# Kernel optimization log

Measured on AMD Instinct MI355X. Metric: run time of the kernel, lower is better.

The kernel has to match this reference:

```python
import jax, jax.numpy as jnp
import numpy as np

RESO = 128

def _prefix_a3(layer, off0):
    # a3[0]=off0; a3[i]=a3[i-1]+2*layer[i-1]+2*layer[i]
    t = jnp.concatenate([jnp.zeros((1,), layer.dtype), 2.0 * layer[:-1] + 2.0 * layer[1:]])
    return off0 + jnp.cumsum(t)

def _prefix_a6(layer, a3):
    # a6[0]=0; a6[i]=a6[i-1]+3*layer[i-1]+layer[i]+2*a3[i-1]
    s = jnp.concatenate([jnp.zeros((1,), layer.dtype), 3.0 * layer[:-1] + layer[1:] + 2.0 * a3[:-1]])
    return jnp.cumsum(s)

def _decode(idx, reso):
    iz = idx % reso                 # selects xLayer channels (0,3)
    iy = (idx // reso) % reso       # selects yLayer channels (1,4)
    ix = idx // (reso * reso)       # selects zLayer channels (2,5)
    return ix, iy, iz

def setup_inputs() -> dict:
    key = jax.random.key(0)
    k1, k2, k3, k4 = jax.random.split(key, 4)
    N = 4194304
    reso = RESO
    ncells = reso ** 3
    renderPointList = jax.random.normal(k1, (N, 3), dtype=jnp.float32) * reso * 0.3 + reso * 0.5
    sdfPointList = jax.random.normal(k2, (N, 3), dtype=jnp.float32) * reso * 0.3 + reso * 0.5
    renderIndexList = jax.random.randint(k3, (N,), 0, ncells, dtype=jnp.int64) if jax.config.jax_enable_x64 else jax.random.randint(k3, (N,), 0, ncells).astype(jnp.int32)
    sdfIndexList = jax.random.randint(k4, (N,), 0, ncells).astype(renderIndexList.dtype)
    xLayer = jnp.ones((reso,), dtype=jnp.float32)
    yLayer = jnp.ones((reso,), dtype=jnp.float32)
    zLayer = jnp.ones((reso,), dtype=jnp.float32)
    c = 1.0 - reso
    offset = jnp.array([2 * c, 2 * c, 2 * c, 3 * c * c - float(reso) ** 2], dtype=jnp.float32)
    return {"renderPointList": renderPointList, "renderIndexList": renderIndexList,
            "sdfPointList": sdfPointList, "sdfIndexList": sdfIndexList,
            "xLayer": xLayer, "yLayer": yLayer, "zLayer": zLayer, "offset": offset}

def reference(renderPointList, renderIndexList, sdfPointList, sdfIndexList, xLayer, yLayer, zLayer, offset):
    reso = xLayer.shape[0]
    xA3 = _prefix_a3(xLayer, offset[0])
    yA4 = _prefix_a3(yLayer, offset[1])
    zA5 = _prefix_a3(zLayer, offset[2])
    xA6 = _prefix_a6(xLayer, xA3)
    yA6 = _prefix_a6(yLayer, yA4)
    zA6 = _prefix_a6(zLayer, zA5)

    # ---- SDF evaluation ----
    ix, iy, iz = _decode(sdfIndexList, reso)
    px, py, pz = sdfPointList[:, 0], sdfPointList[:, 1], sdfPointList[:, 2]
    a0 = xLayer[iz] * px
    a1 = yLayer[iy] * py
    a2 = zLayer[ix] * pz
    a3 = xA3[iz]
    a4 = yA4[iy]
    a5 = zA5[ix]
    a6 = offset[3] + xA6[iz] + yA6[iy] + zA6[ix]
    num = (a0 + a3) * px + (a1 + a4) * py + (a2 + a5) * pz + a6
    den = jnp.sqrt((2 * a0 + a3) ** 2 + (2 * a1 + a4) ** 2 + (2 * a2 + a5) ** 2)
    sdfList = num / den / reso

    # ---- Normal evaluation ----
    jx, jy, jz = _decode(renderIndexList, reso)
    rx, ry, rz = renderPointList[:, 0], renderPointList[:, 1], renderPointList[:, 2]
    nx = 2 * xLayer[jz] * rx + xA3[jz]
    ny = 2 * yLayer[jy] * ry + yA4[jy]
    nz = 2 * zLayer[jx] * rz + zA5[jx]
    n = jnp.stack([nx, ny, nz], axis=1)  # [N,3]
    norm = jnp.sqrt(jnp.sum(n * n, axis=1, keepdims=True))
    normalList = n / jnp.maximum(norm, 1e-12)
    return (sdfList, normalList)
```

## Files before the change

kernel.cpp:

```cpp
#include <hip/hip_runtime.h>

#define RESO 128

__global__ __launch_bounds__(128) void scan_kernel(
    const float* __restrict__ xL, const float* __restrict__ yL,
    const float* __restrict__ zL, const float* __restrict__ off,
    float* __restrict__ ws)
{
    __shared__ float s_tmp[4];
    __shared__ float s_a3[RESO];

    const int tid  = threadIdx.x;
    const int lane = tid & 63;
    const int wave = tid >> 6;

    for (int ax = 0; ax < 3; ++ax) {
        const float* L = (ax == 0) ? xL : (ax == 1) ? yL : zL;
        const float li   = L[tid];
        const float lim1 = (tid > 0) ? L[tid - 1] : 0.f;

        float v = (tid == 0) ? 0.f : 2.f * lim1 + 2.f * li;
        #pragma unroll
        for (int o = 1; o < 64; o <<= 1) {
            float u = __shfl_up(v, o, 64);
            if (lane >= o) v += u;
        }
        if (lane == 63) s_tmp[wave] = v;
        __syncthreads();
        if (wave == 1) v += s_tmp[0];
        const float a3v = off[ax] + v;
        s_a3[tid] = a3v;
        __syncthreads();

        const float a3m1 = (tid > 0) ? s_a3[tid - 1] : 0.f;
        float w = (tid == 0) ? 0.f : 3.f * lim1 + li + 2.f * a3m1;
        #pragma unroll
        for (int o = 1; o < 64; o <<= 1) {
            float u = __shfl_up(w, o, 64);
            if (lane >= o) w += u;
        }
        if (lane == 63) s_tmp[2 + wave] = w;
        __syncthreads();
        if (wave == 1) w += s_tmp[2];

        ws[ax * RESO + tid]       = li;
        ws[(3 + ax) * RESO + tid] = a3v;
        ws[(6 + ax) * RESO + tid] = w;
        __syncthreads();
    }
}

__global__ __launch_bounds__(256) void fused_kernel(
    const float* __restrict__ renderPts, const int* __restrict__ renderIdx,
    const float* __restrict__ sdfPts,    const int* __restrict__ sdfIdx,
    const float* __restrict__ ws,        const float* __restrict__ off,
    float* __restrict__ sdfOut, float* __restrict__ nrmOut, int N)
{
    __shared__ float4 tabS[3][RESO];
    __shared__ float2 tabR[3][RESO];

    const int tid = threadIdx.x;
    if (tid < RESO) {
        #pragma unroll
        for (int ax = 0; ax < 3; ++ax) {
            const float L  = ws[ax * RESO + tid];
            const float a3 = ws[(3 + ax) * RESO + tid];
            const float a6 = ws[(6 + ax) * RESO + tid];
            tabS[ax][tid] = make_float4(L, a3, a6, 0.f);
            tabR[ax][tid] = make_float2(L, a3);
        }
    }
    __syncthreads();

    const float off3 = off[3];
    const int Ng  = N >> 2;
    const int rem = N & 3;
    const int total = Ng + (rem ? 1 : 0);
    const int stride = gridDim.x * blockDim.x;

    for (int t = blockIdx.x * blockDim.x + tid; t < total; t += stride) {
        if (t < Ng) {
            const int4   sid = ((const int4*)sdfIdx)[t];
            const float4 sp0 = ((const float4*)sdfPts)[3 * t + 0];
            const float4 sp1 = ((const float4*)sdfPts)[3 * t + 1];
            const float4 sp2 = ((const float4*)sdfPts)[3 * t + 2];
            const float px[4] = {sp0.x, sp0.w, sp1.z, sp2.y};
            const float py[4] = {sp0.y, sp1.x, sp1.w, sp2.z};
            const float pz[4] = {sp0.z, sp1.y, sp2.x, sp2.w};
            const int  ids[4] = {sid.x, sid.y, sid.z, sid.w};

            float sv[4];
            #pragma unroll
            for (int k = 0; k < 4; ++k) {
                const int id = ids[k];
                const float4 tx = tabS[0][id & 127];
                const float4 ty = tabS[1][(id >> 7) & 127];
                const float4 tz = tabS[2][(id >> 14) & 127];
                const float a0 = tx.x * px[k];
                const float a1 = ty.x * py[k];
                const float a2 = tz.x * pz[k];
                const float a6 = off3 + tx.z + ty.z + tz.z;
                const float num = (a0 + tx.y) * px[k] + (a1 + ty.y) * py[k]
                                + (a2 + tz.y) * pz[k] + a6;
                const float dx = 2.f * a0 + tx.y;
                const float dy = 2.f * a1 + ty.y;
                const float dz = 2.f * a2 + tz.y;
                const float d2 = dx * dx + dy * dy + dz * dz;
                sv[k] = num * __builtin_amdgcn_rsqf(d2) * (1.0f / (float)RESO);
            }
            ((float4*)sdfOut)[t] = make_float4(sv[0], sv[1], sv[2], sv[3]);

            const int4   rid = ((const int4*)renderIdx)[t];
            const float4 rp0 = ((const float4*)renderPts)[3 * t + 0];
            const float4 rp1 = ((const float4*)renderPts)[3 * t + 1];
            const float4 rp2 = ((const float4*)renderPts)[3 * t + 2];
            const float rx[4] = {rp0.x, rp0.w, rp1.z, rp2.y};
            const float ry[4] = {rp0.y, rp1.x, rp1.w, rp2.z};
            const float rz[4] = {rp0.z, rp1.y, rp2.x, rp2.w};
            const int  jds[4] = {rid.x, rid.y, rid.z, rid.w};

            float nx[4], ny[4], nz[4];
            #pragma unroll
            for (int k = 0; k < 4; ++k) {
                const int id = jds[k];
                const float2 ux = tabR[0][id & 127];
                const float2 uy = tabR[1][(id >> 7) & 127];
                const float2 uz = tabR[2][(id >> 14) & 127];
                const float x = 2.f * ux.x * rx[k] + ux.y;
                const float y = 2.f * uy.x * ry[k] + uy.y;
                const float z = 2.f * uz.x * rz[k] + uz.y;
                const float n2 = x * x + y * y + z * z;
                const float inv = __builtin_amdgcn_rsqf(fmaxf(n2, 1e-24f));
                nx[k] = x * inv; ny[k] = y * inv; nz[k] = z * inv;
            }
            float4* no = (float4*)nrmOut;
            no[3 * t + 0] = make_float4(nx[0], ny[0], nz[0], nx[1]);
            no[3 * t + 1] = make_float4(ny[1], nz[1], nx[2], ny[2]);
            no[3 * t + 2] = make_float4(nz[2], nx[3], ny[3], nz[3]);
        } else {
            for (int r = 0; r < rem; ++r) {
                const int i = 4 * Ng + r;
                {
                    const int id = sdfIdx[i];
                    const float4 tx = tabS[0][id & 127];
                    const float4 ty = tabS[1][(id >> 7) & 127];
                    const float4 tz = tabS[2][(id >> 14) & 127];
                    const float px_ = sdfPts[3 * i], py_ = sdfPts[3 * i + 1], pz_ = sdfPts[3 * i + 2];
                    const float a0 = tx.x * px_;
                    const float a1 = ty.x * py_;
                    const float a2 = tz.x * pz_;
                    const float a6 = off3 + tx.z + ty.z + tz.z;
                    const float num = (a0 + tx.y) * px_ + (a1 + ty.y) * py_
                                    + (a2 + tz.y) * pz_ + a6;
                    const float dx = 2.f * a0 + tx.y;
                    const float dy = 2.f * a1 + ty.y;
                    const float dz = 2.f * a2 + tz.y;
                    const float d2 = dx * dx + dy * dy + dz * dz;
                    sdfOut[i] = num * __builtin_amdgcn_rsqf(d2) * (1.0f / (float)RESO);
                }
                {
                    const int id = renderIdx[i];
                    const float2 ux = tabR[0][id & 127];
                    const float2 uy = tabR[1][(id >> 7) & 127];
                    const float2 uz = tabR[2][(id >> 14) & 127];
                    const float rx_ = renderPts[3 * i], ry_ = renderPts[3 * i + 1], rz_ = renderPts[3 * i + 2];
                    const float x = 2.f * ux.x * rx_ + ux.y;
                    const float y = 2.f * uy.x * ry_ + uy.y;
                    const float z = 2.f * uz.x * rz_ + uz.y;
                    const float n2 = x * x + y * y + z * z;
                    const float inv = __builtin_amdgcn_rsqf(fmaxf(n2, 1e-24f));
                    nrmOut[3 * i] = x * inv; nrmOut[3 * i + 1] = y * inv; nrmOut[3 * i + 2] = z * inv;
                }
            }
        }
    }
}

extern "C" void kernel_launch(void* const* d_in, const int* in_sizes, int n_in,
                              void* d_out, int out_size, void* d_ws, size_t ws_size,
                              hipStream_t stream)
{
    const float* renderPts = (const float*)d_in[0];
    const int*   renderIdx = (const int*)d_in[1];
    const float* sdfPts    = (const float*)d_in[2];
    const int*   sdfIdx    = (const int*)d_in[3];
    const float* xL        = (const float*)d_in[4];
    const float* yL        = (const float*)d_in[5];
    const float* zL        = (const float*)d_in[6];
    const float* off       = (const float*)d_in[7];

    float* ws  = (float*)d_ws;
    float* out = (float*)d_out;
    const int N = in_sizes[1];

    scan_kernel<<<1, 128, 0, stream>>>(xL, yL, zL, off, ws);

    fused_kernel<<<2048, 256, 0, stream>>>(renderPts, renderIdx, sdfPts, sdfIdx,
                                           ws, off, out, out + N, N);
}
```

Baseline: 191.7 us.

## Switch to one point per thread with full grid and unified float4 table

Replaces the grid-stride loop that handled four points per thread with 128-bit vector loads and stores by a one-point-per-thread kernel launched over N/256 blocks. Each thread now does scalar strided loads and stores of the xyz triples. The separate float2 render table is dropped and both paths share a single float4 table. This trades vectorized, fewer-instruction memory access for more parallelism and simpler code, but every block must now rebuild the shared table, and the 12-byte-strided scalar accesses may coalesce less efficiently.

```diff
diff --git a/kernel.cpp b/kernel.cpp
--- a/kernel.cpp
+++ b/kernel.cpp
@@ -56,124 +56,58 @@
     const float* __restrict__ ws,        const float* __restrict__ off,
     float* __restrict__ sdfOut, float* __restrict__ nrmOut, int N)
 {
-    __shared__ float4 tabS[3][RESO];
-    __shared__ float2 tabR[3][RESO];
+    __shared__ float4 tab[3][RESO];
 
     const int tid = threadIdx.x;
     if (tid < RESO) {
         #pragma unroll
-        for (int ax = 0; ax < 3; ++ax) {
-            const float L  = ws[ax * RESO + tid];
-            const float a3 = ws[(3 + ax) * RESO + tid];
-            const float a6 = ws[(6 + ax) * RESO + tid];
-            tabS[ax][tid] = make_float4(L, a3, a6, 0.f);
-            tabR[ax][tid] = make_float2(L, a3);
-        }
+        for (int ax = 0; ax < 3; ++ax)
+            tab[ax][tid] = make_float4(ws[ax * RESO + tid],
+                                       ws[(3 + ax) * RESO + tid],
+                                       ws[(6 + ax) * RESO + tid], 0.f);
     }
     __syncthreads();
 
+    const int i = blockIdx.x * blockDim.x + tid;
+    if (i >= N) return;
+
     const float off3 = off[3];
-    const int Ng  = N >> 2;
-    const int rem = N & 3;
-    const int total = Ng + (rem ? 1 : 0);
-    const int stride = gridDim.x * blockDim.x;
 
-    for (int t = blockIdx.x * blockDim.x + tid; t < total; t += stride) {
-        if (t < Ng) {
-            const int4   sid = ((const int4*)sdfIdx)[t];
-            const float4 sp0 = ((const float4*)sdfPts)[3 * t + 0];
-            const float4 sp1 = ((const float4*)sdfPts)[3 * t + 1];
-            const float4 sp2 = ((const float4*)sdfPts)[3 * t + 2];
-            const float px[4] = {sp0.x, sp0.w, sp1.z, sp2.y};
-            const float py[4] = {sp0.y, sp1.x, sp1.w, sp2.z};
-            const float pz[4] = {sp0.z, sp1.y, sp2.x, sp2.w};
-            const int  ids[4] = {sid.x, sid.y, sid.z, sid.w};
+    const int sid = sdfIdx[i];
+    const float px = sdfPts[3 * i + 0];
+    const float py = sdfPts[3 * i + 1];
+    const float pz = sdfPts[3 * i + 2];
+    const float4 tx = tab[0][sid & 127];
+    const float4 ty = tab[1][(sid >> 7) & 127];
+    const float4 tz = tab[2][(sid >> 14) & 127];
 
-            float sv[4];
-            #pragma unroll
-            for (int k = 0; k < 4; ++k) {
-                const int id = ids[k];
-                const float4 tx = tabS[0][id & 127];
-                const float4 ty = tabS[1][(id >> 7) & 127];
-                const float4 tz = tabS[2][(id >> 14) & 127];
-                const float a0 = tx.x * px[k];
-                const float a1 = ty.x * py[k];
-                const float a2 = tz.x * pz[k];
-                const float a6 = off3 + tx.z + ty.z + tz.z;
-                const float num = (a0 + tx.y) * px[k] + (a1 + ty.y) * py[k]
-                                + (a2 + tz.y) * pz[k] + a6;
-                const float dx = 2.f * a0 + tx.y;
-                const float dy = 2.f * a1 + ty.y;
-                const float dz = 2.f * a2 + tz.y;
-                const float d2 = dx * dx + dy * dy + dz * dz;
-                sv[k] = num * __builtin_amdgcn_rsqf(d2) * (1.0f / (float)RESO);
-            }
-            ((float4*)sdfOut)[t] = make_float4(sv[0], sv[1], sv[2], sv[3]);
+    const float a0 = tx.x * px;
+    const float a1 = ty.x * py;
+    const float a2 = tz.x * pz;
+    const float a6 = off3 + tx.z + ty.z + tz.z;
+    const float num = (a0 + tx.y) * px + (a1 + ty.y) * py + (a2 + tz.y) * pz + a6;
+    const float dx = 2.f * a0 + tx.y;
+    const float dy = 2.f * a1 + ty.y;
+    const float dz = 2.f * a2 + tz.y;
+    const float d2 = dx * dx + dy * dy + dz * dz;
+    sdfOut[i] = num * __builtin_amdgcn_rsqf(d2) * (1.0f / (float)RESO);
 
-            const int4   rid = ((const int4*)renderIdx)[t];
-            const float4 rp0 = ((const float4*)renderPts)[3 * t + 0];
-            const float4 rp1 = ((const float4*)renderPts)[3 * t + 1];
-            const float4 rp2 = ((const float4*)renderPts)[3 * t + 2];
-            const float rx[4] = {rp0.x, rp0.w, rp1.z, rp2.y};
-            const float ry[4] = {rp0.y, rp1.x, rp1.w, rp2.z};
-            const float rz[4] = {rp0.z, rp1.y, rp2.x, rp2.w};
-            const int  jds[4] = {rid.x, rid.y, rid.z, rid.w};
+    const int rid = renderIdx[i];
+    const float rx = renderPts[3 * i + 0];
+    const float ry = renderPts[3 * i + 1];
+    const float rz = renderPts[3 * i + 2];
+    const float4 ux = tab[0][rid & 127];
+    const float4 uy = tab[1][(rid >> 7) & 127];
+    const float4 uz = tab[2][(rid >> 14) & 127];
 
-            float nx[4], ny[4], nz[4];
-            #pragma unroll
-            for (int k = 0; k < 4; ++k) {
-                const int id = jds[k];
-                const float2 ux = tabR[0][id & 127];
-                const float2 uy = tabR[1][(id >> 7) & 127];
-                const float2 uz = tabR[2][(id >> 14) & 127];
-                const float x = 2.f * ux.x * rx[k] + ux.y;
-                const float y = 2.f * uy.x * ry[k] + uy.y;
-                const float z = 2.f * uz.x * rz[k] + uz.y;
-                const float n2 = x * x + y * y + z * z;
-                const float inv = __builtin_amdgcn_rsqf(fmaxf(n2, 1e-24f));
-                nx[k] = x * inv; ny[k] = y * inv; nz[k] = z * inv;
-            }
-            float4* no = (float4*)nrmOut;
-            no[3 * t + 0] = make_float4(nx[0], ny[0], nz[0], nx[1]);
-            no[3 * t + 1] = make_float4(ny[1], nz[1], nx[2], ny[2]);
-            no[3 * t + 2] = make_float4(nz[2], nx[3], ny[3], nz[3]);
-        } else {
-            for (int r = 0; r < rem; ++r) {
-                const int i = 4 * Ng + r;
-                {
-                    const int id = sdfIdx[i];
-                    const float4 tx = tabS[0][id & 127];
-                    const float4 ty = tabS[1][(id >> 7) & 127];
-                    const float4 tz = tabS[2][(id >> 14) & 127];
-                    const float px_ = sdfPts[3 * i], py_ = sdfPts[3 * i + 1], pz_ = sdfPts[3 * i + 2];
-                    const float a0 = tx.x * px_;
-                    const float a1 = ty.x * py_;
-                    const float a2 = tz.x * pz_;
-                    const float a6 = off3 + tx.z + ty.z + tz.z;
-                    const float num = (a0 + tx.y) * px_ + (a1 + ty.y) * py_
-                                    + (a2 + tz.y) * pz_ + a6;
-                    const float dx = 2.f * a0 + tx.y;
-                    const float dy = 2.f * a1 + ty.y;
-                    const float dz = 2.f * a2 + tz.y;
-                    const float d2 = dx * dx + dy * dy + dz * dz;
-                    sdfOut[i] = num * __builtin_amdgcn_rsqf(d2) * (1.0f / (float)RESO);
-                }
-                {
-                    const int id = renderIdx[i];
-                    const float2 ux = tabR[0][id & 127];
-                    const float2 uy = tabR[1][(id >> 7) & 127];
-                    const float2 uz = tabR[2][(id >> 14) & 127];
-                    const float rx_ = renderPts[3 * i], ry_ = renderPts[3 * i + 1], rz_ = renderPts[3 * i + 2];
-                    const float x = 2.f * ux.x * rx_ + ux.y;
-                    const float y = 2.f * uy.x * ry_ + uy.y;
-                    const float z = 2.f * uz.x * rz_ + uz.y;
-                    const float n2 = x * x + y * y + z * z;
-                    const float inv = __builtin_amdgcn_rsqf(fmaxf(n2, 1e-24f));
-                    nrmOut[3 * i] = x * inv; nrmOut[3 * i + 1] = y * inv; nrmOut[3 * i + 2] = z * inv;
-                }
-            }
-        }
-    }
+    const float x = 2.f * ux.x * rx + ux.y;
+    const float y = 2.f * uy.x * ry + uy.y;
+    const float z = 2.f * uz.x * rz + uz.y;
+    const float n2 = x * x + y * y + z * z;
+    const float inv = __builtin_amdgcn_rsqf(fmaxf(n2, 1e-24f));
+    nrmOut[3 * i + 0] = x * inv;
+    nrmOut[3 * i + 1] = y * inv;
+    nrmOut[3 * i + 2] = z * inv;
 }
 
 extern "C" void kernel_launch(void* const* d_in, const int* in_sizes, int n_in,
@@ -195,6 +129,8 @@
 
     scan_kernel<<<1, 128, 0, stream>>>(xL, yL, zL, off, ws);
 
-    fused_kernel<<<2048, 256, 0, stream>>>(renderPts, renderIdx, sdfPts, sdfIdx,
-                                           ws, off, out, out + N, N);
+    const int block = 256;
+    const int grid = (N + block - 1) / block;
+    fused_kernel<<<grid, block, 0, stream>>>(renderPts, renderIdx, sdfPts, sdfIdx,
+                                             ws, off, out, out + N, N);
 }
```

After: 187.5 us. 2.2% less time.
